# Kernel optimization log

Measured on AMD Instinct MI355X. Metric: run time of the kernel, lower is better.

Reference implementation:

```python
import jax, jax.numpy as jnp
import numpy as np

N, D, K, V, H, F_ = 4096, 128, 64, 64, 4, 256
EPS = 1e-5


def _layer_norm(x, g, b):
    m = jnp.mean(x, axis=-1, keepdims=True)
    v = jnp.mean((x - m) ** 2, axis=-1, keepdims=True)
    return (x - m) * jax.lax.rsqrt(v + EPS) * g + b


def setup_inputs() -> dict:
    key = jax.random.key(0)
    ks = jax.random.split(key, 20)
    s_in = (2.0 / D) ** 0.5  # kaiming-ish scale for q/k/v projections
    inp = {
        "x": jax.random.normal(ks[0], (N, D), jnp.float32),
        "rpe": jax.random.normal(ks[1], (5, N, N), jnp.float32) * 0.02,
        "Wq": jax.random.normal(ks[2], (H, D, K), jnp.float32) * s_in,
        "bq": jnp.zeros((H, K), jnp.float32),
        "Wk": jax.random.normal(ks[3], (H, D, K), jnp.float32) * s_in,
        "bk": jnp.zeros((H, K), jnp.float32),
        "Wv": jax.random.normal(ks[4], (H, D, V), jnp.float32) * s_in,
        "bv": jnp.zeros((H, V), jnp.float32),
        "rpe_w": jax.random.normal(ks[5], (5,), jnp.float32) * (1.0 / 5.0) ** 0.5,
        "rpe_b": jnp.zeros((), jnp.float32),
        "Wo": jax.random.normal(ks[6], (H * V, D), jnp.float32) * (1.0 / (H * V)) ** 0.5,
        "bo": jnp.zeros((D,), jnp.float32),
        "W1": jax.random.normal(ks[7], (D, F_), jnp.float32) * (1.0 / D) ** 0.5,
        "b1": jnp.zeros((F_,), jnp.float32),
        "W2": jax.random.normal(ks[8], (F_, D), jnp.float32) * (1.0 / F_) ** 0.5,
        "b2": jnp.zeros((D,), jnp.float32),
        "ln1_g": jnp.ones((D,), jnp.float32),
        "ln1_b": jnp.zeros((D,), jnp.float32),
        "ln2_g": jnp.ones((D,), jnp.float32),
        "ln2_b": jnp.zeros((D,), jnp.float32),
    }
    return inp


def reference(x, rpe, Wq, bq, Wk, bk, Wv, bv, rpe_w, rpe_b, Wo, bo,
              W1, b1, W2, b2, ln1_g, ln1_b, ln2_g, ln2_b):
    # ReLU'd per-head projections (vectorized over heads): [H, N, K/V]
    q = jax.nn.relu(jnp.einsum("nd,hdk->hnk", x, Wq) + bq[:, None, :])
    k = jax.nn.relu(jnp.einsum("nd,hdk->hnk", x, Wk) + bk[:, None, :])
    v = jax.nn.relu(jnp.einsum("nd,hdv->hnv", x, Wv) + bv[:, None, :])
    scores = jnp.einsum("hnk,hmk->hnm", q, k) / jnp.sqrt(jnp.asarray(K, x.dtype))
    attn = jax.nn.softmax(scores, axis=-1)  # torch dim=1 on 2D == last axis
    o = jnp.einsum("hnm,hmv->hnv", attn, v)
    mho = jnp.transpose(o, (1, 0, 2)).reshape(N, H * V)  # concat heads
    # RPE: Linear(5->1) over channel axis -> [N, N], then left-matmul
    rpe_weights = jnp.einsum("fnm,f->nm", rpe, rpe_w) + rpe_b
    adjusted = rpe_weights @ mho
    proj = adjusted @ Wo + bo
    x1 = _layer_norm(x + proj, ln1_g, ln1_b)  # dropout is identity (eval)
    ffn = jax.nn.relu(x1 @ W1 + b1) @ W2 + b2
    return _layer_norm(x1 + ffn, ln2_g, ln2_b)
```

## Files before the change

kernel.cpp:

```cpp
#include <hip/hip_runtime.h>

typedef __attribute__((ext_vector_type(8))) short bf16x8;
typedef __attribute__((ext_vector_type(4))) float f32x4;

#define N_TOK 4096
#define NC_ATT 4
#define NC_GEMM 8

static __device__ __forceinline__ ushort f2bf(float f) {
    union { float f; unsigned u; } x; x.f = f;
    unsigned u = x.u;
    unsigned r = (u + 0x7FFFu + ((u >> 16) & 1u)) >> 16;
    return (ushort)r;
}
static __device__ __forceinline__ unsigned pkbf(float a, float b) {
    return (unsigned)f2bf(a) | ((unsigned)f2bf(b) << 16);
}
static __device__ __forceinline__ float bf2f(ushort u) {
    union { unsigned u; float f; } x; x.u = (unsigned)u << 16; return x.f;
}

__global__ void prep_all(const float* __restrict__ x,
                         const float* __restrict__ Wq, const float* __restrict__ Wk,
                         const float* __restrict__ Wv, const float* __restrict__ Wo,
                         const float* __restrict__ W1, const float* __restrict__ W2,
                         ushort* __restrict__ xb, ushort* __restrict__ WqT,
                         ushort* __restrict__ WkT, ushort* __restrict__ WvT,
                         ushort* __restrict__ WoT, ushort* __restrict__ W1T,
                         ushort* __restrict__ W2T) {
    int i = blockIdx.x * 256 + threadIdx.x;
    if (i < 131072) {
        float4 v = ((const float4*)x)[i];
        ushort4 o;
        o.x = f2bf(v.x); o.y = f2bf(v.y); o.z = f2bf(v.z); o.w = f2bf(v.w);
        ((ushort4*)xb)[i] = o;
        return;
    }
    int j = i - 131072;
    int t = j >> 15, e = j & 32767;
    if (t < 3) {
        const float* src = (t == 0 ? Wq : t == 1 ? Wk : Wv);
        ushort* dst = (t == 0 ? WqT : t == 1 ? WkT : WvT);
        int h = e >> 13, rem = e & 8191, d = rem >> 6, k = rem & 63;
        dst[h * 8192 + k * 128 + d] = f2bf(src[e]);
    } else if (t == 3) {
        int r = e >> 7, c = e & 127;
        WoT[c * 256 + r] = f2bf(Wo[e]);
    } else if (t == 4) {
        int r = e >> 8, c = e & 255;
        W1T[c * 128 + r] = f2bf(W1[e]);
    } else {
        int r = e >> 7, c = e & 127;
        W2T[c * 256 + r] = f2bf(W2[e]);
    }
}

__global__ __launch_bounds__(256) void qkv_proj(
    const ushort* __restrict__ xb, const ushort* __restrict__ WqT,
    const ushort* __restrict__ WkT, const ushort* __restrict__ WvT,
    const float* __restrict__ bq, const float* __restrict__ bk, const float* __restrict__ bv,
    ushort* __restrict__ qb, ushort* __restrict__ kb, ushort* __restrict__ vT) {
    int m0 = blockIdx.x * 64;
    int h = blockIdx.y & 3, which = blockIdx.y >> 2;
    int wave = threadIdx.x >> 6, lane = threadIdx.x & 63;
    int fr = lane & 15, kg = lane >> 4;
    int wm = m0 + wave * 16;
    const ushort* WT = (which == 0 ? WqT : which == 1 ? WkT : WvT) + (long)h * 64 * 128;
    const float* bias = (which == 0 ? bq : which == 1 ? bk : bv) + h * 64;
    f32x4 acc[4] = {};
    for (int k0 = 0; k0 < 128; k0 += 32) {
        bf16x8 a = *(const bf16x8*)(xb + (long)(wm + fr) * 128 + k0 + kg * 8);
#pragma unroll
        for (int t = 0; t < 4; ++t) {
            bf16x8 b = *(const bf16x8*)(WT + (long)(t * 16 + fr) * 128 + k0 + kg * 8);
            acc[t] = __builtin_amdgcn_mfma_f32_16x16x32_bf16(a, b, acc[t], 0, 0, 0);
        }
    }
    int rb = wm + kg * 4;
#pragma unroll
    for (int t = 0; t < 4; ++t) {
        int col = t * 16 + fr;
        float bs = bias[col];
        if (which == 2) {
            ushort4 o;
            o.x = f2bf(fmaxf(acc[t][0] + bs, 0.f));
            o.y = f2bf(fmaxf(acc[t][1] + bs, 0.f));
            o.z = f2bf(fmaxf(acc[t][2] + bs, 0.f));
            o.w = f2bf(fmaxf(acc[t][3] + bs, 0.f));
            *(ushort4*)(vT + ((long)h * 64 + col) * N_TOK + rb) = o;
        } else {
            ushort* dst = (which == 0 ? qb : kb) + (long)h * N_TOK * 64;
            float scl = (which == 0) ? 0.125f * 1.44269504f : 1.0f;
#pragma unroll
            for (int r = 0; r < 4; ++r)
                dst[(long)(rb + r) * 64 + col] = f2bf(fmaxf(acc[t][r] + bs, 0.f) * scl);
        }
    }
}

__global__ __launch_bounds__(256) void attn_flash2(
    const ushort* __restrict__ qb, const ushort* __restrict__ kb,
    const ushort* __restrict__ vT, ushort* __restrict__ opart,
    float* __restrict__ mlpart) {
    int qt = blockIdx.x, h = blockIdx.y, cz = blockIdx.z;
    int w = threadIdx.x >> 6, lane = threadIdx.x & 63;
    int fr = lane & 15, kg = lane >> 4;
    int lr = lane >> 3, lc = lane & 7;
    int swz = (lc ^ (lr & 7)) * 8;
    __shared__ ushort Kt[2][64 * 64];
    __shared__ ushort Vt[2][64 * 64];
    __shared__ ushort Pl[4][16 * 64];
    const ushort* qh = qb + (long)h * N_TOK * 64;
    const ushort* kh = kb + (long)h * N_TOK * 64;
    const ushort* vh = vT + (long)h * 64 * N_TOK;
    int q0 = qt * 64 + w * 16;
    bf16x8 qf0 = *(const bf16x8*)(qh + (long)(q0 + fr) * 64 + kg * 8);
    bf16x8 qf1 = *(const bf16x8*)(qh + (long)(q0 + fr) * 64 + 32 + kg * 8);
    f32x4 o[4] = {};
    float mrun = -1e30f, lrun = 0.f;
    int nbase = cz * (N_TOK / NC_ATT);
    auto stage = [&](int buf, int s) {
        int n0 = nbase + s * 64;
#pragma unroll
        for (int j = 0; j < 2; ++j) {
            int i = w * 2 + j;
            int row = i * 8 + lr;
            __builtin_amdgcn_global_load_lds(
                (const __attribute__((address_space(1))) unsigned int*)(kh + (long)(n0 + row) * 64 + swz),
                (__attribute__((address_space(3))) unsigned int*)(&Kt[buf][i * 512]), 16, 0, 0);
        }
#pragma unroll
        for (int j = 0; j < 2; ++j) {
            int i = w * 2 + j;
            int row = i * 8 + lr;
            __builtin_amdgcn_global_load_lds(
                (const __attribute__((address_space(1))) unsigned int*)(vh + (long)row * N_TOK + n0 + swz),
                (__attribute__((address_space(3))) unsigned int*)(&Vt[buf][i * 512]), 16, 0, 0);
        }
    };
    stage(0, 0);
    __syncthreads();
    const int NS = (N_TOK / NC_ATT) / 64;
    for (int s = 0; s < NS; ++s) {
        int buf = s & 1;
        if (s + 1 < NS) stage(buf ^ 1, s + 1);
        f32x4 sc[4] = {};
#pragma unroll
        for (int t = 0; t < 4; ++t) {
            int row = t * 16 + fr;
            bf16x8 k0 = *(const bf16x8*)(&Kt[buf][row * 64 + ((kg * 8) ^ ((row & 7) * 8))]);
            bf16x8 k1 = *(const bf16x8*)(&Kt[buf][row * 64 + ((32 + kg * 8) ^ ((row & 7) * 8))]);
            sc[t] = __builtin_amdgcn_mfma_f32_16x16x32_bf16(k0, qf0, sc[t], 0, 0, 0);
            sc[t] = __builtin_amdgcn_mfma_f32_16x16x32_bf16(k1, qf1, sc[t], 0, 0, 0);
        }
        float mx = sc[0][0];
#pragma unroll
        for (int t = 0; t < 4; ++t)
#pragma unroll
            for (int r = 0; r < 4; ++r) mx = fmaxf(mx, sc[t][r]);
        mx = fmaxf(mx, __shfl_xor(mx, 16));
        mx = fmaxf(mx, __shfl_xor(mx, 32));
        if (__any(mx - mrun > 8.f)) {
            float mnew = fmaxf(mrun, mx);
            float alpha = exp2f(mrun - mnew);
            lrun *= alpha;
            mrun = mnew;
            float aq[4];
#pragma unroll
            for (int r = 0; r < 4; ++r) aq[r] = __shfl(alpha, kg * 4 + r);
#pragma unroll
            for (int t = 0; t < 4; ++t)
#pragma unroll
                for (int r = 0; r < 4; ++r) o[t][r] *= aq[r];
        }
        float rs = 0.f;
#pragma unroll
        for (int t = 0; t < 4; ++t)
#pragma unroll
            for (int r = 0; r < 4; ++r) {
                float p = exp2f(sc[t][r] - mrun);
                sc[t][r] = p;
                rs += p;
            }
        rs += __shfl_xor(rs, 16);
        rs += __shfl_xor(rs, 32);
        lrun += rs;
#pragma unroll
        for (int t = 0; t < 4; ++t) {
            uint2 u;
            u.x = pkbf(sc[t][0], sc[t][1]);
            u.y = pkbf(sc[t][2], sc[t][3]);
            *(uint2*)(&Pl[w][fr * 64 + ((t * 16 + kg * 4) ^ ((fr & 7) * 8))]) = u;
        }
#pragma unroll
        for (int ks = 0; ks < 2; ++ks) {
            bf16x8 pf = *(const bf16x8*)(&Pl[w][fr * 64 + ((ks * 32 + kg * 8) ^ ((fr & 7) * 8))]);
#pragma unroll
            for (int t = 0; t < 4; ++t) {
                int row = t * 16 + fr;
                bf16x8 b = *(const bf16x8*)(&Vt[buf][row * 64 + ((ks * 32 + kg * 8) ^ ((row & 7) * 8))]);
                o[t] = __builtin_amdgcn_mfma_f32_16x16x32_bf16(pf, b, o[t], 0, 0, 0);
            }
        }
        __syncthreads();
    }
    float linv = 1.0f / lrun;
    float lq[4];
#pragma unroll
    for (int r = 0; r < 4; ++r) lq[r] = __shfl(linv, kg * 4 + r);
    ushort* ob = opart + (((long)cz * 4 + h) * N_TOK + q0 + kg * 4) * 64;
#pragma unroll
    for (int t = 0; t < 4; ++t)
#pragma unroll
        for (int r = 0; r < 4; ++r)
            ob[(long)r * 64 + t * 16 + fr] = f2bf(o[t][r] * lq[r]);
    if (lane < 16) {
        float* mlb = mlpart + (((long)cz * 4 + h) * N_TOK + q0 + lane) * 2;
        mlb[0] = mrun;
        mlb[1] = lrun;
    }
}

__global__ __launch_bounds__(256) void combine_wo(
    const ushort* __restrict__ opart, const float* __restrict__ mlpart,
    const ushort* __restrict__ WoT, ushort* __restrict__ PT) {
    int q0 = blockIdx.x * 64;
    int tid = threadIdx.x;
    __shared__ ushort mt[64 * 256];
    {
        int q = tid >> 2, vg = tid & 3;
        long qg = q0 + q;
#pragma unroll
        for (int h = 0; h < 4; ++h) {
            float m[NC_ATT], l[NC_ATT], M = -1e30f;
#pragma unroll
            for (int c = 0; c < NC_ATT; ++c) {
                const float* mlb = mlpart + (((long)c * 4 + h) * N_TOK + qg) * 2;
                m[c] = mlb[0]; l[c] = mlb[1];
                M = fmaxf(M, m[c]);
            }
            float L = 0.f, co[NC_ATT];
#pragma unroll
            for (int c = 0; c < NC_ATT; ++c) { co[c] = exp2f(m[c] - M) * l[c]; L += co[c]; }
            float inv = 1.0f / L;
#pragma unroll
            for (int c = 0; c < NC_ATT; ++c) co[c] *= inv;
            float a[16];
#pragma unroll
            for (int j = 0; j < 16; ++j) a[j] = 0.f;
#pragma unroll
            for (int c = 0; c < NC_ATT; ++c) {
                const ushort* pr = opart + (((long)c * 4 + h) * N_TOK + qg) * 64 + vg * 16;
                bf16x8 v0 = *(const bf16x8*)(pr);
                bf16x8 v1 = *(const bf16x8*)(pr + 8);
#pragma unroll
                for (int j = 0; j < 8; ++j) {
                    a[j] += co[c] * bf2f((ushort)v0[j]);
                    a[8 + j] += co[c] * bf2f((ushort)v1[j]);
                }
            }
            int c0 = h * 64 + vg * 16;
            uint2 u0, u1;
            u0.x = pkbf(a[0], a[1]); u0.y = pkbf(a[2], a[3]);
            u1.x = pkbf(a[4], a[5]); u1.y = pkbf(a[6], a[7]);
            *(uint2*)(&mt[q * 256 + (c0 ^ ((q & 7) * 8))]) = u0;
            *(uint2*)(&mt[q * 256 + ((c0 + 4) ^ ((q & 7) * 8))]) = u1;
            u0.x = pkbf(a[8], a[9]); u0.y = pkbf(a[10], a[11]);
            u1.x = pkbf(a[12], a[13]); u1.y = pkbf(a[14], a[15]);
            *(uint2*)(&mt[q * 256 + ((c0 + 8) ^ ((q & 7) * 8))]) = u0;
            *(uint2*)(&mt[q * 256 + ((c0 + 12) ^ ((q & 7) * 8))]) = u1;
        }
    }
    __syncthreads();
    {
        int w = tid >> 6, lane = tid & 63;
        int fr = lane & 15, kg = lane >> 4;
        f32x4 acc[2][4] = {};
        for (int k0 = 0; k0 < 256; k0 += 32) {
            bf16x8 a0 = *(const bf16x8*)(WoT + (long)(w * 32 + fr) * 256 + k0 + kg * 8);
            bf16x8 a1 = *(const bf16x8*)(WoT + (long)(w * 32 + 16 + fr) * 256 + k0 + kg * 8);
#pragma unroll
            for (int qt = 0; qt < 4; ++qt) {
                int row = qt * 16 + fr;
                bf16x8 b = *(const bf16x8*)(&mt[row * 256 + ((k0 + kg * 8) ^ ((row & 7) * 8))]);
                acc[0][qt] = __builtin_amdgcn_mfma_f32_16x16x32_bf16(a0, b, acc[0][qt], 0, 0, 0);
                acc[1][qt] = __builtin_amdgcn_mfma_f32_16x16x32_bf16(a1, b, acc[1][qt], 0, 0, 0);
            }
        }
#pragma unroll
        for (int dt = 0; dt < 2; ++dt)
#pragma unroll
            for (int qt = 0; qt < 4; ++qt)
#pragma unroll
                for (int r = 0; r < 4; ++r)
                    PT[(long)(w * 32 + dt * 16 + kg * 4 + r) * N_TOK + q0 + qt * 16 + fr] =
                        f2bf(acc[dt][qt][r]);
    }
}

__global__ __launch_bounds__(512) void gemm_big_fused(
    const float* __restrict__ rpe, const float* __restrict__ rpe_w,
    const float* __restrict__ rpe_b, const ushort* __restrict__ PT,
    float* __restrict__ part) {
    int mt = blockIdx.x, cz = blockIdx.y;
    int tid = threadIdx.x;
    int w = tid >> 6, lane = tid & 63;
    int fr = lane & 15, kg = lane >> 4;
    int lr = lane >> 3, lc = lane & 7;
    int swz = (lc ^ (lr & 7)) * 8;
    int ms = w >> 1, nh = w & 1;
    __shared__ ushort Bt[2][128 * 64];
    __shared__ ushort At[2][64 * 64];
    int m0 = mt * 64;
    long kbase = (long)cz * (N_TOK / NC_GEMM);
    float w0 = rpe_w[0], w1 = rpe_w[1], w2 = rpe_w[2], w3 = rpe_w[3], w4 = rpe_w[4];
    float bb = rpe_b[0];
    auto stage_B = [&](int buf, int s) {
        const ushort* src = PT + kbase + s * 64 + swz;
#pragma unroll
        for (int j = 0; j < 2; ++j) {
            int i = w * 2 + j;
            int row = i * 8 + lr;
            __builtin_amdgcn_global_load_lds(
                (const __attribute__((address_space(1))) unsigned int*)(src + (long)row * N_TOK),
                (__attribute__((address_space(3))) unsigned int*)(&Bt[buf][i * 512]), 16, 0, 0);
        }
    };
    float4 pA[10];
    auto load_A = [&](int s) {
        const float* base = rpe + (long)m0 * N_TOK + kbase + s * 64;
#pragma unroll
        for (int rnd = 0; rnd < 2; ++rnd) {
            int idx = tid + rnd * 512;
            int row = idx >> 4, c4 = (idx & 15) * 4;
            const float* pr = base + (long)row * N_TOK + c4;
#pragma unroll
            for (int pl = 0; pl < 5; ++pl)
                pA[rnd * 5 + pl] = *(const float4*)(pr + (long)pl * ((long)N_TOK * N_TOK));
        }
    };
    auto write_A = [&](int buf) {
#pragma unroll
        for (int rnd = 0; rnd < 2; ++rnd) {
            int idx = tid + rnd * 512;
            int row = idx >> 4, c4 = (idx & 15) * 4;
            float4 p0 = pA[rnd * 5], p1 = pA[rnd * 5 + 1], p2 = pA[rnd * 5 + 2];
            float4 p3 = pA[rnd * 5 + 3], p4 = pA[rnd * 5 + 4];
            float v0 = bb + w0 * p0.x + w1 * p1.x + w2 * p2.x + w3 * p3.x + w4 * p4.x;
            float v1 = bb + w0 * p0.y + w1 * p1.y + w2 * p2.y + w3 * p3.y + w4 * p4.y;
            float v2 = bb + w0 * p0.z + w1 * p1.z + w2 * p2.z + w3 * p3.z + w4 * p4.z;
            float v3 = bb + w0 * p0.w + w1 * p1.w + w2 * p2.w + w3 * p3.w + w4 * p4.w;
            uint2 u;
            u.x = pkbf(v0, v1);
            u.y = pkbf(v2, v3);
            *(uint2*)(&At[buf][row * 64 + (c4 ^ ((row & 7) * 8))]) = u;
        }
    };
    f32x4 acc[4] = {};
    load_A(0);
    stage_B(0, 0);
    write_A(0);
    __syncthreads();
    const int NS = (N_TOK / NC_GEMM) / 64;
    int arow = ms * 16 + fr;
    for (int s = 0; s < NS; ++s) {
        int buf = s & 1;
        if (s + 1 < NS) { stage_B(buf ^ 1, s + 1); load_A(s + 1); }
#pragma unroll
        for (int ks = 0; ks < 2; ++ks) {
            bf16x8 av = *(const bf16x8*)(&At[buf][arow * 64 + ((ks * 32 + kg * 8) ^ ((arow & 7) * 8))]);
#pragma unroll
            for (int nf = 0; nf < 4; ++nf) {
                int row = nh * 64 + nf * 16 + fr;
                bf16x8 b = *(const bf16x8*)(&Bt[buf][row * 64 + ((ks * 32 + kg * 8) ^ ((row & 7) * 8))]);
                acc[nf] = __builtin_amdgcn_mfma_f32_16x16x32_bf16(av, b, acc[nf], 0, 0, 0);
            }
        }
        if (s + 1 < NS) write_A(buf ^ 1);
        __syncthreads();
    }
    float* pb = part + ((long)cz * N_TOK + m0 + ms * 16 + kg * 4) * 128 + nh * 64 + fr;
#pragma unroll
    for (int nf = 0; nf < 4; ++nf)
#pragma unroll
        for (int r = 0; r < 4; ++r)
            pb[(long)r * 128 + nf * 16] = acc[nf][r];
}

__global__ __launch_bounds__(256) void megatail(
    const float* __restrict__ gpart, const float* __restrict__ bo,
    const float* __restrict__ x, const float* __restrict__ g1,
    const float* __restrict__ lb1, const ushort* __restrict__ W1T,
    const float* __restrict__ b1, const ushort* __restrict__ W2T,
    const float* __restrict__ b2, const float* __restrict__ g2,
    const float* __restrict__ lb2, float* __restrict__ out) {
    int r0 = blockIdx.x * 16;
    int tid = threadIdx.x;
    int w = tid >> 6, lane = tid & 63;
    int fr = lane & 15, kg = lane >> 4;
    __shared__ float x1f[16][132];
    __shared__ ushort x1b[16][128];
    __shared__ ushort hbuf[16][256];
    __shared__ float otile[16][132];
    int row = tid >> 4, c0 = (tid & 15) * 8;
    {
        float v[8];
        float4 s0 = {0.f, 0.f, 0.f, 0.f}, s1 = {0.f, 0.f, 0.f, 0.f};
#pragma unroll
        for (int c = 0; c < NC_GEMM; ++c) {
            const float* pr = gpart + ((long)c * N_TOK + r0 + row) * 128 + c0;
            float4 a = *(const float4*)(pr);
            float4 b = *(const float4*)(pr + 4);
            s0.x += a.x; s0.y += a.y; s0.z += a.z; s0.w += a.w;
            s1.x += b.x; s1.y += b.y; s1.z += b.z; s1.w += b.w;
        }
        const float* xr = x + (long)(r0 + row) * 128 + c0;
        v[0] = s0.x + bo[c0 + 0] + xr[0];
        v[1] = s0.y + bo[c0 + 1] + xr[1];
        v[2] = s0.z + bo[c0 + 2] + xr[2];
        v[3] = s0.w + bo[c0 + 3] + xr[3];
        v[4] = s1.x + bo[c0 + 4] + xr[4];
        v[5] = s1.y + bo[c0 + 5] + xr[5];
        v[6] = s1.z + bo[c0 + 6] + xr[6];
        v[7] = s1.w + bo[c0 + 7] + xr[7];
        float s = 0.f;
#pragma unroll
        for (int jj = 0; jj < 8; ++jj) s += v[jj];
#pragma unroll
        for (int off = 1; off < 16; off <<= 1) s += __shfl_xor(s, off);
        float mean = s * (1.0f / 128.0f);
        float ss = 0.f;
#pragma unroll
        for (int jj = 0; jj < 8; ++jj) { float d = v[jj] - mean; ss += d * d; }
#pragma unroll
        for (int off = 1; off < 16; off <<= 1) ss += __shfl_xor(ss, off);
        float rstd = rsqrtf(ss * (1.0f / 128.0f) + 1e-5f);
        union { bf16x8 vec; ushort us[8]; } pk8;
#pragma unroll
        for (int jj = 0; jj < 8; ++jj) {
            float y = (v[jj] - mean) * rstd * g1[c0 + jj] + lb1[c0 + jj];
            x1f[row][c0 + jj] = y;
            pk8.us[jj] = f2bf(y);
        }
        *(bf16x8*)(&x1b[row][c0 ^ ((row & 7) * 8)]) = pk8.vec;
    }
    __syncthreads();
    {
        f32x4 a1[4] = {};
#pragma unroll
        for (int ks = 0; ks < 4; ++ks) {
            bf16x8 a = *(const bf16x8*)(&x1b[fr][(ks * 32 + kg * 8) ^ ((fr & 7) * 8)]);
#pragma unroll
            for (int t = 0; t < 4; ++t) {
                bf16x8 b = *(const bf16x8*)(W1T + (long)(w * 64 + t * 16 + fr) * 128 + ks * 32 + kg * 8);
                a1[t] = __builtin_amdgcn_mfma_f32_16x16x32_bf16(a, b, a1[t], 0, 0, 0);
            }
        }
#pragma unroll
        for (int t = 0; t < 4; ++t) {
            int col = w * 64 + t * 16 + fr;
            float bs = b1[col];
#pragma unroll
            for (int r = 0; r < 4; ++r) {
                int rr = kg * 4 + r;
                hbuf[rr][col ^ ((rr & 7) * 8)] = f2bf(fmaxf(a1[t][r] + bs, 0.f));
            }
        }
    }
    __syncthreads();
    {
        f32x4 a2[2] = {};
#pragma unroll
        for (int ks = 0; ks < 8; ++ks) {
            bf16x8 a = *(const bf16x8*)(&hbuf[fr][(ks * 32 + kg * 8) ^ ((fr & 7) * 8)]);
#pragma unroll
            for (int t = 0; t < 2; ++t) {
                bf16x8 b = *(const bf16x8*)(W2T + (long)(w * 32 + t * 16 + fr) * 256 + ks * 32 + kg * 8);
                a2[t] = __builtin_amdgcn_mfma_f32_16x16x32_bf16(a, b, a2[t], 0, 0, 0);
            }
        }
#pragma unroll
        for (int t = 0; t < 2; ++t) {
            int col = w * 32 + t * 16 + fr;
            float bs = b2[col];
#pragma unroll
            for (int r = 0; r < 4; ++r) {
                int rr = kg * 4 + r;
                otile[rr][col] = a2[t][r] + bs + x1f[rr][col];
            }
        }
    }
    __syncthreads();
    {
        float v[8];
        float s = 0.f;
#pragma unroll
        for (int jj = 0; jj < 8; ++jj) { v[jj] = otile[row][c0 + jj]; s += v[jj]; }
#pragma unroll
        for (int off = 1; off < 16; off <<= 1) s += __shfl_xor(s, off);
        float mean = s * (1.0f / 128.0f);
        float ss = 0.f;
#pragma unroll
        for (int jj = 0; jj < 8; ++jj) { float d = v[jj] - mean; ss += d * d; }
#pragma unroll
        for (int off = 1; off < 16; off <<= 1) ss += __shfl_xor(ss, off);
        float rstd = rsqrtf(ss * (1.0f / 128.0f) + 1e-5f);
#pragma unroll
        for (int jj = 0; jj < 8; ++jj) {
            float y = (v[jj] - mean) * rstd * g2[c0 + jj] + lb2[c0 + jj];
            out[(long)(r0 + row) * 128 + c0 + jj] = y;
        }
    }
}

extern "C" void kernel_launch(void* const* d_in, const int* in_sizes, int n_in,
                              void* d_out, int out_size, void* d_ws, size_t ws_size,
                              hipStream_t stream) {
    const float* x     = (const float*)d_in[0];
    const float* rpe   = (const float*)d_in[1];
    const float* Wq    = (const float*)d_in[2];
    const float* bq    = (const float*)d_in[3];
    const float* Wk    = (const float*)d_in[4];
    const float* bk    = (const float*)d_in[5];
    const float* Wv    = (const float*)d_in[6];
    const float* bv    = (const float*)d_in[7];
    const float* rpe_w = (const float*)d_in[8];
    const float* rpe_b = (const float*)d_in[9];
    const float* Wo    = (const float*)d_in[10];
    const float* bo    = (const float*)d_in[11];
    const float* W1    = (const float*)d_in[12];
    const float* b1    = (const float*)d_in[13];
    const float* W2    = (const float*)d_in[14];
    const float* b2    = (const float*)d_in[15];
    const float* g1    = (const float*)d_in[16];
    const float* lb1   = (const float*)d_in[17];
    const float* g2    = (const float*)d_in[18];
    const float* lb2   = (const float*)d_in[19];

    char* wp = (char*)d_ws;
    auto alloc = [&](size_t sz) { char* p = wp; wp += (sz + 255) & ~(size_t)255; return p; };
    ushort* xb    = (ushort*)alloc((size_t)4096 * 128 * 2);
    ushort* WqT   = (ushort*)alloc((size_t)4 * 64 * 128 * 2);
    ushort* WkT   = (ushort*)alloc((size_t)4 * 64 * 128 * 2);
    ushort* WvT   = (ushort*)alloc((size_t)4 * 64 * 128 * 2);
    ushort* WoT   = (ushort*)alloc((size_t)128 * 256 * 2);
    ushort* W1T   = (ushort*)alloc((size_t)256 * 128 * 2);
    ushort* W2T   = (ushort*)alloc((size_t)128 * 256 * 2);
    ushort* qb    = (ushort*)alloc((size_t)4 * 4096 * 64 * 2);
    ushort* kbuf  = (ushort*)alloc((size_t)4 * 4096 * 64 * 2);
    ushort* vT    = (ushort*)alloc((size_t)4 * 64 * 4096 * 2);
    ushort* PTb   = (ushort*)alloc((size_t)128 * 4096 * 2);
    ushort* opart = (ushort*)alloc((size_t)NC_ATT * 4 * 4096 * 64 * 2);
    float*  mlprt = (float*)alloc((size_t)NC_ATT * 4 * 4096 * 2 * 4);
    float*  gpart = (float*)alloc((size_t)NC_GEMM * 4096 * 128 * 4);

    prep_all<<<1280, 256, 0, stream>>>(x, Wq, Wk, Wv, Wo, W1, W2,
                                       xb, WqT, WkT, WvT, WoT, W1T, W2T);
    qkv_proj<<<dim3(64, 12), 256, 0, stream>>>(xb, WqT, WkT, WvT, bq, bk, bv, qb, kbuf, vT);
    attn_flash2<<<dim3(64, 4, NC_ATT), 256, 0, stream>>>(qb, kbuf, vT, opart, mlprt);
    combine_wo<<<64, 256, 0, stream>>>(opart, mlprt, WoT, PTb);
    gemm_big_fused<<<dim3(64, NC_GEMM), 512, 0, stream>>>(rpe, rpe_w, rpe_b, PTb, gpart);
    megatail<<<256, 256, 0, stream>>>(gpart, bo, x, g1, lb1, W1T, b1, W2T, b2,
                                      g2, lb2, (float*)d_out);
}
```

Baseline: 151.6 us.

## Restructure RPE GEMM A-loading into large batched phases; shrink combine_wo tiles

combine_wo now handles 16 queries per block instead of 64, launching 256 blocks so more CUs are busy, with each thread covering one head slice. In gemm_big_fused, the per-step register-prefetched A tile (64x64) is replaced by two phases that each load and reduce a 64x256 slab of the five RPE planes into a single LDS buffer. Each thread issues ten float4 loads per round, putting more bytes in flight against the dominant 5xNxN fp32 stream. The trade-off is that the A loads are no longer overlapped with MFMA work across steps, and extra barriers are added.

After: 148.8 us. Within noise of the previous version (-1.8%).

```diff
diff --git a/kernel.cpp b/kernel.cpp
--- a/kernel.cpp
+++ b/kernel.cpp
@@ -224,77 +224,67 @@
 __global__ __launch_bounds__(256) void combine_wo(
     const ushort* __restrict__ opart, const float* __restrict__ mlpart,
     const ushort* __restrict__ WoT, ushort* __restrict__ PT) {
-    int q0 = blockIdx.x * 64;
+    int q0 = blockIdx.x * 16;
     int tid = threadIdx.x;
-    __shared__ ushort mt[64 * 256];
+    __shared__ ushort mt[16 * 256];
     {
-        int q = tid >> 2, vg = tid & 3;
+        int q = tid >> 4, cg = tid & 15;
+        int h = cg >> 2;
         long qg = q0 + q;
-#pragma unroll
-        for (int h = 0; h < 4; ++h) {
-            float m[NC_ATT], l[NC_ATT], M = -1e30f;
-#pragma unroll
-            for (int c = 0; c < NC_ATT; ++c) {
-                const float* mlb = mlpart + (((long)c * 4 + h) * N_TOK + qg) * 2;
-                m[c] = mlb[0]; l[c] = mlb[1];
-                M = fmaxf(M, m[c]);
-            }
-            float L = 0.f, co[NC_ATT];
-#pragma unroll
-            for (int c = 0; c < NC_ATT; ++c) { co[c] = exp2f(m[c] - M) * l[c]; L += co[c]; }
-            float inv = 1.0f / L;
-#pragma unroll
-            for (int c = 0; c < NC_ATT; ++c) co[c] *= inv;
-            float a[16];
-#pragma unroll
-            for (int j = 0; j < 16; ++j) a[j] = 0.f;
-#pragma unroll
-            for (int c = 0; c < NC_ATT; ++c) {
-                const ushort* pr = opart + (((long)c * 4 + h) * N_TOK + qg) * 64 + vg * 16;
-                bf16x8 v0 = *(const bf16x8*)(pr);
-                bf16x8 v1 = *(const bf16x8*)(pr + 8);
-#pragma unroll
-                for (int j = 0; j < 8; ++j) {
-                    a[j] += co[c] * bf2f((ushort)v0[j]);
-                    a[8 + j] += co[c] * bf2f((ushort)v1[j]);
-                }
-            }
-            int c0 = h * 64 + vg * 16;
-            uint2 u0, u1;
-            u0.x = pkbf(a[0], a[1]); u0.y = pkbf(a[2], a[3]);
-            u1.x = pkbf(a[4], a[5]); u1.y = pkbf(a[6], a[7]);
-            *(uint2*)(&mt[q * 256 + (c0 ^ ((q & 7) * 8))]) = u0;
-            *(uint2*)(&mt[q * 256 + ((c0 + 4) ^ ((q & 7) * 8))]) = u1;
-            u0.x = pkbf(a[8], a[9]); u0.y = pkbf(a[10], a[11]);
-            u1.x = pkbf(a[12], a[13]); u1.y = pkbf(a[14], a[15]);
-            *(uint2*)(&mt[q * 256 + ((c0 + 8) ^ ((q & 7) * 8))]) = u0;
-            *(uint2*)(&mt[q * 256 + ((c0 + 12) ^ ((q & 7) * 8))]) = u1;
+        float m[NC_ATT], l[NC_ATT], M = -1e30f;
+#pragma unroll
+        for (int c = 0; c < NC_ATT; ++c) {
+            const float* mlb = mlpart + (((long)c * 4 + h) * N_TOK + qg) * 2;
+            m[c] = mlb[0]; l[c] = mlb[1];
+            M = fmaxf(M, m[c]);
+        }
+        float L = 0.f, co[NC_ATT];
+#pragma unroll
+        for (int c = 0; c < NC_ATT; ++c) { co[c] = exp2f(m[c] - M) * l[c]; L += co[c]; }
+        float inv = 1.0f / L;
+#pragma unroll
+        for (int c = 0; c < NC_ATT; ++c) co[c] *= inv;
+        float a[16];
+#pragma unroll
+        for (int j = 0; j < 16; ++j) a[j] = 0.f;
+#pragma unroll
+        for (int c = 0; c < NC_ATT; ++c) {
+            const ushort* pr = opart + (((long)c * 4 + h) * N_TOK + qg) * 64 + (cg & 3) * 16;
+            bf16x8 v0 = *(const bf16x8*)(pr);
+            bf16x8 v1 = *(const bf16x8*)(pr + 8);
+#pragma unroll
+            for (int j = 0; j < 8; ++j) {
+                a[j] += co[c] * bf2f((ushort)v0[j]);
+                a[8 + j] += co[c] * bf2f((ushort)v1[j]);
+            }
+        }
+        int c0 = cg * 16;
+#pragma unroll
+        for (int g = 0; g < 4; ++g) {
+            uint2 u;
+            u.x = pkbf(a[g * 4 + 0], a[g * 4 + 1]);
+            u.y = pkbf(a[g * 4 + 2], a[g * 4 + 3]);
+            *(uint2*)(&mt[q * 256 + ((c0 + g * 4) ^ ((q & 7) * 8))]) = u;
         }
     }
     __syncthreads();
     {
         int w = tid >> 6, lane = tid & 63;
         int fr = lane & 15, kg = lane >> 4;
-        f32x4 acc[2][4] = {};
+        f32x4 acc[2] = {};
         for (int k0 = 0; k0 < 256; k0 += 32) {
             bf16x8 a0 = *(const bf16x8*)(WoT + (long)(w * 32 + fr) * 256 + k0 + kg * 8);
             bf16x8 a1 = *(const bf16x8*)(WoT + (long)(w * 32 + 16 + fr) * 256 + k0 + kg * 8);
-#pragma unroll
-            for (int qt = 0; qt < 4; ++qt) {
-                int row = qt * 16 + fr;
-                bf16x8 b = *(const bf16x8*)(&mt[row * 256 + ((k0 + kg * 8) ^ ((row & 7) * 8))]);
-                acc[0][qt] = __builtin_amdgcn_mfma_f32_16x16x32_bf16(a0, b, acc[0][qt], 0, 0, 0);
-                acc[1][qt] = __builtin_amdgcn_mfma_f32_16x16x32_bf16(a1, b, acc[1][qt], 0, 0, 0);
-            }
+            bf16x8 b = *(const bf16x8*)(&mt[fr * 256 + ((k0 + kg * 8) ^ ((fr & 7) * 8))]);
+            acc[0] = __builtin_amdgcn_mfma_f32_16x16x32_bf16(a0, b, acc[0], 0, 0, 0);
+            acc[1] = __builtin_amdgcn_mfma_f32_16x16x32_bf16(a1, b, acc[1], 0, 0, 0);
         }
 #pragma unroll
         for (int dt = 0; dt < 2; ++dt)
 #pragma unroll
-            for (int qt = 0; qt < 4; ++qt)
-#pragma unroll
-                for (int r = 0; r < 4; ++r)
-                    PT[(long)(w * 32 + dt * 16 + kg * 4 + r) * N_TOK + q0 + qt * 16 + fr] =
-                        f2bf(acc[dt][qt][r]);
+            for (int r = 0; r < 4; ++r)
+                PT[(long)(w * 32 + dt * 16 + kg * 4 + r) * N_TOK + q0 + fr] =
+                    f2bf(acc[dt][r]);
     }
 }
 
@@ -307,16 +297,19 @@
     int w = tid >> 6, lane = tid & 63;
     int fr = lane & 15, kg = lane >> 4;
     int lr = lane >> 3, lc = lane & 7;
-    int swz = (lc ^ (lr & 7)) * 8;
+    int swzB = (lc ^ (lr & 7)) * 8;
     int ms = w >> 1, nh = w & 1;
+    __shared__ ushort At[64 * 256];
     __shared__ ushort Bt[2][128 * 64];
-    __shared__ ushort At[2][64 * 64];
     int m0 = mt * 64;
     long kbase = (long)cz * (N_TOK / NC_GEMM);
     float w0 = rpe_w[0], w1 = rpe_w[1], w2 = rpe_w[2], w3 = rpe_w[3], w4 = rpe_w[4];
     float bb = rpe_b[0];
-    auto stage_B = [&](int buf, int s) {
-        const ushort* src = PT + kbase + s * 64 + swz;
+    const long PLANE = (long)N_TOK * N_TOK;
+    int arow = ms * 16 + fr;
+    int lrow = tid >> 3, seg = tid & 7;
+    auto stage_B = [&](int buf, int sb) {
+        const ushort* src = PT + kbase + sb * 64 + swzB;
 #pragma unroll
         for (int j = 0; j < 2; ++j) {
             int i = w * 2 + j;
@@ -326,58 +319,49 @@
                 (__attribute__((address_space(3))) unsigned int*)(&Bt[buf][i * 512]), 16, 0, 0);
         }
     };
-    float4 pA[10];
-    auto load_A = [&](int s) {
-        const float* base = rpe + (long)m0 * N_TOK + kbase + s * 64;
-#pragma unroll
-        for (int rnd = 0; rnd < 2; ++rnd) {
-            int idx = tid + rnd * 512;
-            int row = idx >> 4, c4 = (idx & 15) * 4;
-            const float* pr = base + (long)row * N_TOK + c4;
-#pragma unroll
-            for (int pl = 0; pl < 5; ++pl)
-                pA[rnd * 5 + pl] = *(const float4*)(pr + (long)pl * ((long)N_TOK * N_TOK));
-        }
-    };
-    auto write_A = [&](int buf) {
-#pragma unroll
-        for (int rnd = 0; rnd < 2; ++rnd) {
-            int idx = tid + rnd * 512;
-            int row = idx >> 4, c4 = (idx & 15) * 4;
-            float4 p0 = pA[rnd * 5], p1 = pA[rnd * 5 + 1], p2 = pA[rnd * 5 + 2];
-            float4 p3 = pA[rnd * 5 + 3], p4 = pA[rnd * 5 + 4];
-            float v0 = bb + w0 * p0.x + w1 * p1.x + w2 * p2.x + w3 * p3.x + w4 * p4.x;
-            float v1 = bb + w0 * p0.y + w1 * p1.y + w2 * p2.y + w3 * p3.y + w4 * p4.y;
-            float v2 = bb + w0 * p0.z + w1 * p1.z + w2 * p2.z + w3 * p3.z + w4 * p4.z;
-            float v3 = bb + w0 * p0.w + w1 * p1.w + w2 * p2.w + w3 * p3.w + w4 * p4.w;
-            uint2 u;
-            u.x = pkbf(v0, v1);
-            u.y = pkbf(v2, v3);
-            *(uint2*)(&At[buf][row * 64 + (c4 ^ ((row & 7) * 8))]) = u;
-        }
-    };
     f32x4 acc[4] = {};
-    load_A(0);
-    stage_B(0, 0);
-    write_A(0);
-    __syncthreads();
-    const int NS = (N_TOK / NC_GEMM) / 64;
-    int arow = ms * 16 + fr;
-    for (int s = 0; s < NS; ++s) {
-        int buf = s & 1;
-        if (s + 1 < NS) { stage_B(buf ^ 1, s + 1); load_A(s + 1); }
-#pragma unroll
-        for (int ks = 0; ks < 2; ++ks) {
-            bf16x8 av = *(const bf16x8*)(&At[buf][arow * 64 + ((ks * 32 + kg * 8) ^ ((arow & 7) * 8))]);
-#pragma unroll
-            for (int nf = 0; nf < 4; ++nf) {
-                int row = nh * 64 + nf * 16 + fr;
-                bf16x8 b = *(const bf16x8*)(&Bt[buf][row * 64 + ((ks * 32 + kg * 8) ^ ((row & 7) * 8))]);
-                acc[nf] = __builtin_amdgcn_mfma_f32_16x16x32_bf16(av, b, acc[nf], 0, 0, 0);
-            }
-        }
-        if (s + 1 < NS) write_A(buf ^ 1);
+    for (int p = 0; p < 2; ++p) {
+        if (p == 0) stage_B(0, 0);
+        const float* base = rpe + (long)(m0 + lrow) * N_TOK + kbase + p * 256;
+#pragma unroll
+        for (int rnd = 0; rnd < 4; ++rnd) {
+            float4 pv[2][5];
+#pragma unroll
+            for (int g = 0; g < 2; ++g) {
+                int col = (seg + (rnd * 2 + g) * 8) * 4;
+#pragma unroll
+                for (int pl = 0; pl < 5; ++pl)
+                    pv[g][pl] = *(const float4*)(base + col + pl * PLANE);
+            }
+#pragma unroll
+            for (int g = 0; g < 2; ++g) {
+                int col = (seg + (rnd * 2 + g) * 8) * 4;
+                float4 a0 = pv[g][0], a1 = pv[g][1], a2 = pv[g][2], a3 = pv[g][3], a4 = pv[g][4];
+                uint2 u;
+                u.x = pkbf(bb + w0 * a0.x + w1 * a1.x + w2 * a2.x + w3 * a3.x + w4 * a4.x,
+                           bb + w0 * a0.y + w1 * a1.y + w2 * a2.y + w3 * a3.y + w4 * a4.y);
+                u.y = pkbf(bb + w0 * a0.z + w1 * a1.z + w2 * a2.z + w3 * a3.z + w4 * a4.z,
+                           bb + w0 * a0.w + w1 * a1.w + w2 * a2.w + w3 * a3.w + w4 * a4.w);
+                *(uint2*)(&At[lrow * 256 + (col ^ ((lrow & 7) * 8))]) = u;
+            }
+        }
         __syncthreads();
+        for (int ks = 0; ks < 4; ++ks) {
+            int sb = p * 4 + ks;
+            if (sb + 1 < 8) stage_B((sb + 1) & 1, sb + 1);
+#pragma unroll
+            for (int k2 = 0; k2 < 2; ++k2) {
+                int c = ks * 64 + k2 * 32 + kg * 8;
+                bf16x8 av = *(const bf16x8*)(&At[arow * 256 + (c ^ ((arow & 7) * 8))]);
+#pragma unroll
+                for (int nf = 0; nf < 4; ++nf) {
+                    int row = nh * 64 + nf * 16 + fr;
+                    bf16x8 b = *(const bf16x8*)(&Bt[sb & 1][row * 64 + ((k2 * 32 + kg * 8) ^ ((row & 7) * 8))]);
+                    acc[nf] = __builtin_amdgcn_mfma_f32_16x16x32_bf16(av, b, acc[nf], 0, 0, 0);
+                }
+            }
+            __syncthreads();
+        }
     }
     float* pb = part + ((long)cz * N_TOK + m0 + ms * 16 + kg * 4) * 128 + nh * 64 + fr;
 #pragma unroll
@@ -558,7 +542,7 @@
                                        xb, WqT, WkT, WvT, WoT, W1T, W2T);
     qkv_proj<<<dim3(64, 12), 256, 0, stream>>>(xb, WqT, WkT, WvT, bq, bk, bv, qb, kbuf, vT);
     attn_flash2<<<dim3(64, 4, NC_ATT), 256, 0, stream>>>(qb, kbuf, vT, opart, mlprt);
-    combine_wo<<<64, 256, 0, stream>>>(opart, mlprt, WoT, PTb);
+    combine_wo<<<256, 256, 0, stream>>>(opart, mlprt, WoT, PTb);
     gemm_big_fused<<<dim3(64, NC_GEMM), 512, 0, stream>>>(rpe, rpe_w, rpe_b, PTb, gpart);
     megatail<<<256, 256, 0, stream>>>(gpart, bo, x, g1, lb1, W1T, b1, W2T, b2,
                                       g2, lb2, (float*)d_out);
```
